# Kernel tuning notes

Hardware: AMD Instinct MI355X
Metric: run time of the kernel (lower is better)

## Reference

```python
import jax, jax.numpy as jnp
import numpy as np

N, C, H, W = 4, 128, 128, 128
G, K, PAD, DIL = 4, 3, 1, 1
P = K * K
HID = 4 * C
EPS = 1e-6


def ln(x, w, b):
    m = jnp.mean(x, -1, keepdims=True)
    v = jnp.mean((x - m) ** 2, -1, keepdims=True)
    return (x - m) * jax.lax.rsqrt(v + EPS) * w + b


def linear(x, w, b):
    return x @ w.T + b


def grid_sample_zeros(img, grid):
    # img: (B,Hi,Wi,Cc); grid: (B,L,P,2) xy in [-1,1]; bilinear, zeros padding, align_corners=False
    B, Hi, Wi, Cc = img.shape
    gx = (grid[..., 0] + 1.0) * (Wi * 0.5) - 0.5
    gy = (grid[..., 1] + 1.0) * (Hi * 0.5) - 0.5
    x0 = jnp.floor(gx)
    y0 = jnp.floor(gy)
    wx1 = gx - x0
    wy1 = gy - y0
    flat = img.reshape(B, Hi * Wi, Cc)
    Bq, L, Pq = gx.shape

    def tap(yy, xx, wgt):
        valid = (xx >= 0) & (xx <= Wi - 1) & (yy >= 0) & (yy <= Hi - 1)
        idx = (jnp.clip(yy, 0, Hi - 1) * Wi + jnp.clip(xx, 0, Wi - 1)).astype(jnp.int32)
        v = jnp.take_along_axis(flat, idx.reshape(B, L * Pq)[..., None], axis=1)
        return v.reshape(B, L, Pq, Cc) * (wgt * valid)[..., None]

    return (tap(y0, x0, (1 - wx1) * (1 - wy1))
            + tap(y0, x0 + 1, wx1 * (1 - wy1))
            + tap(y0 + 1, x0, (1 - wx1) * wy1)
            + tap(y0 + 1, x0 + 1, wx1 * wy1))


def dcn_core(x, offset, mask):
    # faithful port of dcnv3_core_pytorch (stride=1, offset_scale=1.0)
    n, h, w, c = x.shape
    gc = c // G
    xp = jnp.pad(x, ((0, 0), (PAD, PAD), (PAD, PAD), (0, 0)))
    hi, wi = h + 2 * PAD, w + 2 * PAD
    base = (DIL * (K - 1)) // 2 + 0.5
    ref_y = (base + jnp.arange(h, dtype=jnp.float32)) / hi
    ref_x = (base + jnp.arange(w, dtype=jnp.float32)) / wi
    ref = jnp.stack([jnp.broadcast_to(ref_x[None, :], (h, w)),
                     jnp.broadcast_to(ref_y[:, None], (h, w))], -1)  # (h,w,2) xy
    ks = jnp.arange(K, dtype=jnp.float32) * DIL - (DIL * (K - 1)) // 2
    gxk, gyk = jnp.meshgrid(ks, ks, indexing='ij')  # x slow, y fast (torch meshgrid order)
    grid = jnp.tile(jnp.stack([gxk / wi, gyk / hi], -1).reshape(P, 2), (G, 1))  # (G*P,2)
    sn = jnp.array([wi, hi], jnp.float32)
    loc = ref[None, :, :, None, :] + grid[None, None, None] + offset.reshape(n, h, w, G * P, 2) / sn
    sg = (2.0 * loc - 1.0).reshape(n, h * w, G, P, 2).transpose(0, 2, 1, 3, 4).reshape(n * G, h * w, P, 2)
    img = xp.reshape(n, hi, wi, G, gc).transpose(0, 3, 1, 2, 4).reshape(n * G, hi, wi, gc)
    samp = grid_sample_zeros(img, sg)  # (n*G, h*w, P, gc)
    m = mask.reshape(n, h * w, G, P).transpose(0, 2, 1, 3).reshape(n * G, h * w, P)
    out = jnp.einsum('blpc,blp->blc', samp, m)
    return out.reshape(n, G, h * w, gc).transpose(0, 2, 1, 3).reshape(n, h, w, c)


def dcn_forward(xcl, dw_w, dw_b, dwln_w, dwln_b, off_w, off_b, mask_w, mask_b, outproj_w, outproj_b):
    n, h, w, c = xcl.shape
    y = jax.lax.conv_general_dilated(xcl.transpose(0, 3, 1, 2), dw_w, (1, 1),
                                     ((PAD, PAD), (PAD, PAD)),
                                     dimension_numbers=('NCHW', 'OIHW', 'NCHW'),
                                     feature_group_count=C)
    y = y + dw_b[None, :, None, None]
    x1 = jax.nn.gelu(ln(y.transpose(0, 2, 3, 1), dwln_w, dwln_b), approximate=False)
    offset = linear(x1, off_w, off_b)
    m = jax.nn.softmax(linear(x1, mask_w, mask_b).reshape(n, h, w, G, P), -1).reshape(n, h, w, G * P)
    out = dcn_core(x1, offset, m)
    return linear(out, outproj_w, outproj_b)


def setup_inputs():
    key = jax.random.key(0)
    ks = jax.random.split(key, 8)
    s = 0.02
    return {
        "x": jax.random.normal(ks[0], (N, C, H, W), jnp.float32),
        "norm1_w": jnp.ones((C,), jnp.float32), "norm1_b": jnp.zeros((C,), jnp.float32),
        "dw_w": jax.random.normal(ks[1], (C, 1, K, K), jnp.float32) * 0.1,
        "dw_b": jnp.zeros((C,), jnp.float32),
        "dwln_w": jnp.ones((C,), jnp.float32), "dwln_b": jnp.zeros((C,), jnp.float32),
        "off_w": jax.random.normal(ks[2], (G * P * 2, C), jnp.float32) * 0.05,
        "off_b": jax.random.normal(ks[3], (G * P * 2,), jnp.float32) * 0.5,
        "mask_w": jax.random.normal(ks[4], (G * P, C), jnp.float32) * 0.05,
        "mask_b": jnp.zeros((G * P,), jnp.float32),
        "outproj_w": jax.random.normal(ks[5], (C, C), jnp.float32) * s,
        "outproj_b": jnp.zeros((C,), jnp.float32),
        "norm2_w": jnp.ones((C,), jnp.float32), "norm2_b": jnp.zeros((C,), jnp.float32),
        "fc1_w": jax.random.normal(ks[6], (HID, C), jnp.float32) * s,
        "fc1_b": jnp.zeros((HID,), jnp.float32),
        "fc2_w": jax.random.normal(ks[7], (C, HID), jnp.float32) * s,
        "fc2_b": jnp.zeros((C,), jnp.float32),
    }


def reference(x, norm1_w, norm1_b, dw_w, dw_b, dwln_w, dwln_b, off_w, off_b,
              mask_w, mask_b, outproj_w, outproj_b, norm2_w, norm2_b,
              fc1_w, fc1_b, fc2_w, fc2_b):
    # pre-norm branch (layer_scale=None, post_norm=False, res_post_norm=False, drop_path=Identity)
    xcl = ln(x.transpose(0, 2, 3, 1), norm1_w, norm1_b)  # channels_first -> channels_last LN
    d = dcn_forward(xcl, dw_w, dw_b, dwln_w, dwln_b, off_w, off_b, mask_w, mask_b, outproj_w, outproj_b)
    x = x + d.transpose(0, 3, 1, 2)
    y = ln(x.transpose(0, 2, 3, 1), norm2_w, norm2_b)
    y = linear(jax.nn.gelu(linear(y, fc1_w, fc1_b), approximate=False), fc2_w, fc2_b)
    return x + y.transpose(0, 3, 1, 2)
```

## Files before the change

### kernel.cpp

```cpp
#include <hip/hip_runtime.h>

typedef unsigned short ushort_t;
typedef short short8 __attribute__((ext_vector_type(8)));
typedef float f32x4 __attribute__((ext_vector_type(4)));
typedef ushort_t ushort8v __attribute__((ext_vector_type(8)));
typedef ushort_t ushort4v __attribute__((ext_vector_type(4)));

#define HWsz 16384
#define NHWsz 65536
#define YS 136

__device__ __forceinline__ float b2f(ushort_t u){ return __uint_as_float(((unsigned)u)<<16); }
__device__ __forceinline__ ushort_t f2b(float f){
  unsigned x = __float_as_uint(f);
  x += 0x7fffu + ((x>>16)&1u);
  return (ushort_t)(x>>16);
}
__device__ __forceinline__ float gelu_fast(float x){
  float t = x*x;
  float e = __expf(x*(1.5957691216f + 0.0713548163f*t));
  return x - x*__builtin_amdgcn_rcpf(1.0f + e);
}

#define HSW(p, b) ((p)*1024 + ((b) ^ (((p)&7)<<4)))
#define XSW(p, b) ((p)*256  + ((b) ^ (((p)&7)<<4)))

__global__ __launch_bounds__(256) void kW_cvt(const float* __restrict__ w1, const float* __restrict__ w2,
    const float* __restrict__ offw, const float* __restrict__ maskw, const float* __restrict__ dww,
    const float* __restrict__ pw, const float* __restrict__ offb, const float* __restrict__ mb,
    ushort_t* __restrict__ w1b, ushort_t* __restrict__ w2b, ushort_t* __restrict__ owmb,
    float* __restrict__ dwwT, ushort_t* __restrict__ pwh, ushort_t* __restrict__ pwl,
    float* __restrict__ obm){
  int i = blockIdx.x*256 + threadIdx.x;
  w1b[i] = f2b(w1[i]);
  w2b[i] = f2b(w2[i]);
  if (i < 16384){
    int row = i >> 7, k = i & 127;
    float v = 0.f;
    if (row < 72) v = offw[row*128 + k];
    else if (row < 108) v = maskw[(row-72)*128 + k];
    owmb[i] = f2b(v);
    float pv = pw[i];
    ushort_t hi = f2b(pv);
    pwh[i] = hi;
    pwl[i] = f2b(pv - b2f(hi));
  }
  if (i < 1152){
    int k = i >> 7, c = i & 127;
    dwwT[i] = dww[c*9 + k];
  }
  if (i < 128){
    obm[i] = (i < 72) ? offb[i] : ((i < 108) ? mb[i-72] : 0.f);
  }
}

__global__ __launch_bounds__(256) void kA_ln1(const float* __restrict__ x,
    const float* __restrict__ w, const float* __restrict__ b,
    ushort_t* __restrict__ xcl){
  __shared__ float tile[128*66];
  __shared__ float psum[256], psq[256];
  __shared__ float ms[64], rs[64];
  int t = threadIdx.x;
  int pos0 = blockIdx.x * 64;
  int n = pos0 >> 14, hw0 = pos0 & 16383;
  const float* xb = x + (size_t)n*128*HWsz + hw0;
  for (int i=0;i<32;i++){
    int e = i*256+t;
    int c = e>>6, p = e&63;
    tile[c*66+p] = xb[(size_t)c*HWsz + p];
  }
  __syncthreads();
  {
    int part = t>>6, p = t&63;
    float s=0.f, q=0.f;
    for (int c=part*32; c<part*32+32; c++){ float v = tile[c*66+p]; s+=v; q+=v*v; }
    psum[part*64+p]=s; psq[part*64+p]=q;
  }
  __syncthreads();
  if (t<64){
    float s=psum[t]+psum[64+t]+psum[128+t]+psum[192+t];
    float q=psq[t]+psq[64+t]+psq[128+t]+psq[192+t];
    float m = s*(1.0f/128.0f);
    float v = q*(1.0f/128.0f)-m*m;
    ms[t]=m; rs[t]=rsqrtf(v+1e-6f);
  }
  __syncthreads();
  for (int i=0;i<32;i++){
    int e = i*256+t;
    int p = e>>7, c = e&127;
    float v = (tile[c*66+p]-ms[p])*rs[p]*w[c]+b[c];
    xcl[(size_t)(pos0+p)*128 + c] = f2b(v);
  }
}

__global__ __launch_bounds__(256) void kB_dw(const ushort_t* __restrict__ xcl,
    const float* __restrict__ dwwT, const float* __restrict__ dwb,
    const float* __restrict__ lnw, const float* __restrict__ lnb,
    ushort_t* __restrict__ x1){
  __shared__ float partS[16*17], partQ[16*17];
  __shared__ float ms[16], rs[16];
  int t = threadIdx.x;
  int pos0 = blockIdx.x*16;
  int n = pos0>>14, hw0 = pos0&16383, h = hw0>>7, w0 = hw0&127;
  int pp = t>>4, l = t&15, ch0 = l*8;
  int w = w0 + pp;
  float acc[8];
  {
    float4 b0 = *(const float4*)(dwb + ch0);
    float4 b1 = *(const float4*)(dwb + ch0 + 4);
    acc[0]=b0.x; acc[1]=b0.y; acc[2]=b0.z; acc[3]=b0.w;
    acc[4]=b1.x; acc[5]=b1.y; acc[6]=b1.z; acc[7]=b1.w;
  }
  #pragma unroll
  for (int kh=0; kh<3; kh++){
    int hy = h + kh - 1;
    if ((unsigned)hy < 128u){
      #pragma unroll
      for (int kw=0; kw<3; kw++){
        int wx = w + kw - 1;
        if ((unsigned)wx < 128u){
          ushort8v xv = *(const ushort8v*)(xcl + ((size_t)(n*16384 + hy*128 + wx))*128 + ch0);
          const float* wr = dwwT + (kh*3+kw)*128 + ch0;
          float4 w0v = *(const float4*)(wr);
          float4 w1v = *(const float4*)(wr+4);
          acc[0] += b2f(xv[0])*w0v.x; acc[1] += b2f(xv[1])*w0v.y;
          acc[2] += b2f(xv[2])*w0v.z; acc[3] += b2f(xv[3])*w0v.w;
          acc[4] += b2f(xv[4])*w1v.x; acc[5] += b2f(xv[5])*w1v.y;
          acc[6] += b2f(xv[6])*w1v.z; acc[7] += b2f(xv[7])*w1v.w;
        }
      }
    }
  }
  {
    float s=0.f, q=0.f;
    #pragma unroll
    for (int j=0;j<8;j++){ s+=acc[j]; q+=acc[j]*acc[j]; }
    partS[pp*17+l]=s; partQ[pp*17+l]=q;
  }
  __syncthreads();
  {
    int p = t>>4, j = t&15;
    float s = partS[p*17+j];
    float q = partQ[p*17+j];
    s += __shfl_xor(s, 1);  q += __shfl_xor(q, 1);
    s += __shfl_xor(s, 2);  q += __shfl_xor(q, 2);
    s += __shfl_xor(s, 4);  q += __shfl_xor(q, 4);
    s += __shfl_xor(s, 8);  q += __shfl_xor(q, 8);
    if (j == 0){
      float m = s*(1.0f/128.0f);
      float var = q*(1.0f/128.0f) - m*m;
      ms[p]=m; rs[p]=rsqrtf(var+1e-6f);
    }
  }
  __syncthreads();
  {
    float m = ms[pp], r = rs[pp];
    float4 lw0 = *(const float4*)(lnw + ch0);
    float4 lw1 = *(const float4*)(lnw + ch0 + 4);
    float4 lb0 = *(const float4*)(lnb + ch0);
    float4 lb1 = *(const float4*)(lnb + ch0 + 4);
    float lw[8] = {lw0.x,lw0.y,lw0.z,lw0.w,lw1.x,lw1.y,lw1.z,lw1.w};
    float lb[8] = {lb0.x,lb0.y,lb0.z,lb0.w,lb1.x,lb1.y,lb1.z,lb1.w};
    ushort8v o;
    #pragma unroll
    for (int j=0;j<8;j++){
      float v = (acc[j]-m)*r*lw[j]+lb[j];
      o[j] = f2b(gelu_fast(v));
    }
    *(ushort8v*)(x1 + (size_t)(pos0+pp)*128 + ch0) = o;
  }
}

#define RS 120
__global__ __launch_bounds__(256) void kCD_dcn(const ushort_t* __restrict__ x1,
    const ushort_t* __restrict__ owmb, const float* __restrict__ obm,
    ushort_t* __restrict__ dcnout){
  __shared__ __align__(16) ushort_t xLb[16*YS];
  __shared__ float raw[16*RS];
  __shared__ __align__(16) float descW[576*4];
  __shared__ __align__(16) int   descO[576*4];
  int t = threadIdx.x;
  int pos0 = blockIdx.x*16;
  int n = pos0>>14, hw0 = pos0&16383, h = hw0>>7, w0 = hw0&127;
  const size_t imgbase = (size_t)n*16384*128;

  *(ushort8v*)(xLb + (t>>4)*YS + (t&15)*8) = *(const ushort8v*)(x1 + (size_t)pos0*128 + t*8);
  __syncthreads();

  {
    int wave = t>>6, lane = t&63;
    int ma = lane&15, quad = lane>>4;
    short8 afrag[4];
    #pragma unroll
    for (int ks=0; ks<4; ks++)
      afrag[ks] = *(const short8*)(xLb + ma*YS + ks*32 + quad*8);
    f32x4 acc[2];
    acc[0] = (f32x4){0.f,0.f,0.f,0.f};
    acc[1] = (f32x4){0.f,0.f,0.f,0.f};
    #pragma unroll
    for (int tile=0; tile<2; tile++){
      const ushort_t* brow = owmb + (size_t)(wave*32 + tile*16 + ma)*128 + quad*8;
      #pragma unroll
      for (int ks=0; ks<4; ks++){
        short8 bfrag = *(const short8*)(brow + ks*32);
        acc[tile] = __builtin_amdgcn_mfma_f32_16x16x32_bf16(bfrag, afrag[ks], acc[tile], 0,0,0);
      }
    }
    #pragma unroll
    for (int tile=0; tile<2; tile++){
      int row0 = wave*32 + tile*16 + quad*4;
      if (row0 < 112){
        f32x4 bias4 = *(const f32x4*)(obm + row0);
        f32x4 o;
        #pragma unroll
        for (int r=0;r<4;r++) o[r] = acc[tile][r] + bias4[r];
        *(f32x4*)(raw + ma*RS + row0) = o;
      }
    }
  }
  __syncthreads();

  if (t < 64){
    int p = t>>2, g = t&3;
    float* mr = raw + p*RS + 72 + g*9;
    float mx = -1e30f;
    for (int q=0;q<9;q++) mx = fmaxf(mx, mr[q]);
    float e[9]; float ssum=0.f;
    for (int q=0;q<9;q++){ e[q]=expf(mr[q]-mx); ssum+=e[q]; }
    float inv = 1.0f/ssum;
    for (int q=0;q<9;q++) mr[q] = e[q]*inv;
  }
  __syncthreads();

  for (int it=0; it<3; it++){
    int tid = t + 256*it;
    if (tid < 576){
      int pp = tid/36, rem = tid - pp*36;
      int g = rem/9, p = rem - g*9;
      int i = p/3, j = p - i*3;
      float ox = raw[pp*RS + 2*(g*9+p)];
      float oy = raw[pp*RS + 2*(g*9+p)+1];
      float mval = raw[pp*RS + 72 + g*9 + p];
      float px = (float)(w0 + pp + i - 1) + ox;
      float py = (float)(h + j - 1) + oy;
      float fx0 = floorf(px), fy0 = floorf(py);
      int ix0 = (int)fx0, iy0 = (int)fy0;
      float fx = px - fx0, fy = py - fy0;
      float vx0 = ((unsigned)ix0     < 128u) ? 1.f : 0.f;
      float vx1 = ((unsigned)(ix0+1) < 128u) ? 1.f : 0.f;
      float vy0 = ((unsigned)iy0     < 128u) ? 1.f : 0.f;
      float vy1 = ((unsigned)(iy0+1) < 128u) ? 1.f : 0.f;
      int cx0 = min(max(ix0,0),127), cx1 = min(max(ix0+1,0),127);
      int cy0 = min(max(iy0,0),127), cy1 = min(max(iy0+1,0),127);
      float4 wv;
      wv.x = (1.f-fx)*(1.f-fy)*mval*vx0*vy0;
      wv.y = fx*(1.f-fy)*mval*vx1*vy0;
      wv.z = (1.f-fx)*fy*mval*vx0*vy1;
      wv.w = fx*fy*mval*vx1*vy1;
      int4 ov;
      ov.x = (cy0*128+cx0)*128;
      ov.y = (cy0*128+cx1)*128;
      ov.z = (cy1*128+cx0)*128;
      ov.w = (cy1*128+cx1)*128;
      *(float4*)(descW + tid*4) = wv;
      *(int4*)(descO + tid*4) = ov;
    }
  }
  __syncthreads();

  {
    int pp = t>>4, l = t&15;
    int ch0 = l*8, g = l>>2;
    const ushort_t* ib = x1 + imgbase + ch0;
    float acc[8];
    #pragma unroll
    for (int j=0;j<8;j++) acc[j]=0.f;
    int dbase = pp*36 + g*9;
    #pragma unroll
    for (int p=0;p<9;p++){
      float4 wv = *(const float4*)(descW + (dbase+p)*4);
      int4  ov = *(const int4*)(descO + (dbase+p)*4);
      ushort8v v00 = *(const ushort8v*)(ib + ov.x);
      ushort8v v10 = *(const ushort8v*)(ib + ov.y);
      ushort8v v01 = *(const ushort8v*)(ib + ov.z);
      ushort8v v11 = *(const ushort8v*)(ib + ov.w);
      #pragma unroll
      for (int j=0;j<8;j++){
        float s = wv.x*b2f(v00[j]) + wv.y*b2f(v10[j]) + wv.z*b2f(v01[j]) + wv.w*b2f(v11[j]);
        acc[j] += s;
      }
    }
    ushort8v outv;
    #pragma unroll
    for (int j=0;j<8;j++) outv[j] = f2b(acc[j]);
    *(ushort8v*)(dcnout + (size_t)(pos0+pp)*128 + ch0) = outv;
  }
}

__global__ __launch_bounds__(256, 4) void kEFG(const ushort_t* __restrict__ dcnout,
    const ushort_t* __restrict__ pwh, const ushort_t* __restrict__ pwl,
    const float* __restrict__ pb, const float* __restrict__ x,
    const float* __restrict__ n2w, const float* __restrict__ n2b,
    const ushort_t* __restrict__ w1b, const float* __restrict__ b1,
    const ushort_t* __restrict__ w2b, const float* __restrict__ b2,
    float* __restrict__ out){
  __shared__ __align__(16) char hidb[32*1024];
  __shared__ __align__(16) char xnb[32*256];
  float* partS = (float*)hidb;
  float* partQ = partS + 32*17;
  float* msh   = partQ + 32*17;
  float* rsh   = msh + 32;

  int t = threadIdx.x;
  int pos0 = blockIdx.x*32;
  int n = pos0>>14, hw0 = pos0&16383;
  int wave = t>>6, lane = t&63;
  int ma = lane&15, quad = lane>>4;

  short8 af[2][4];
  #pragma unroll
  for (int mt=0; mt<2; mt++)
    #pragma unroll
    for (int ks=0; ks<4; ks++)
      af[mt][ks] = *(const short8*)(dcnout + (size_t)(pos0+mt*16+ma)*128 + ks*32 + quad*8);

  float res[2][2][4];
  #pragma unroll
  for (int tile=0; tile<2; tile++){
    int c0 = wave*32 + tile*16 + quad*4;
    #pragma unroll
    for (int mt=0; mt<2; mt++){
      int p = mt*16 + ma;
      #pragma unroll
      for (int r=0;r<4;r++)
        res[tile][mt][r] = x[((size_t)(n*128) + c0 + r)*HWsz + hw0 + p];
    }
  }

  f32x4 acc[2][2];
  #pragma unroll
  for (int i=0;i<2;i++){ acc[i][0]=(f32x4){0.f,0.f,0.f,0.f}; acc[i][1]=(f32x4){0.f,0.f,0.f,0.f}; }
  #pragma unroll
  for (int tile=0; tile<2; tile++){
    int c0 = wave*32 + tile*16;
    const ushort_t* bh = pwh + (size_t)(c0 + ma)*128 + quad*8;
    const ushort_t* bl = pwl + (size_t)(c0 + ma)*128 + quad*8;
    #pragma unroll
    for (int ks=0; ks<4; ks++){
      short8 bfh = *(const short8*)(bh + ks*32);
      short8 bfl = *(const short8*)(bl + ks*32);
      #pragma unroll
      for (int mt=0; mt<2; mt++){
        acc[tile][mt] = __builtin_amdgcn_mfma_f32_16x16x32_bf16(bfh, af[mt][ks], acc[tile][mt], 0,0,0);
        acc[tile][mt] = __builtin_amdgcn_mfma_f32_16x16x32_bf16(bfl, af[mt][ks], acc[tile][mt], 0,0,0);
      }
    }
  }

  float vb[2][2][4];
  float sAcc[2], qAcc[2];
  sAcc[0]=0.f; sAcc[1]=0.f; qAcc[0]=0.f; qAcc[1]=0.f;
  #pragma unroll
  for (int tile=0; tile<2; tile++){
    int c0 = wave*32 + tile*16 + quad*4;
    f32x4 bias4 = *(const f32x4*)(pb + c0);
    #pragma unroll
    for (int mt=0; mt<2; mt++){
      #pragma unroll
      for (int r=0;r<4;r++){
        float v = acc[tile][mt][r] + bias4[r] + res[tile][mt][r];
        float vv = b2f(f2b(v));
        vb[tile][mt][r] = vv;
        sAcc[mt] += vv; qAcc[mt] += vv*vv;
      }
    }
  }
  #pragma unroll
  for (int mt=0; mt<2; mt++){
    int p = mt*16 + ma;
    partS[p*17 + wave*4 + quad] = sAcc[mt];
    partQ[p*17 + wave*4 + quad] = qAcc[mt];
  }
  __syncthreads();
  {
    int p = t>>3, j = t&7;
    float s = partS[p*17 + 2*j] + partS[p*17 + 2*j + 1];
    float q = partQ[p*17 + 2*j] + partQ[p*17 + 2*j + 1];
    s += __shfl_xor(s, 1);  q += __shfl_xor(q, 1);
    s += __shfl_xor(s, 2);  q += __shfl_xor(q, 2);
    s += __shfl_xor(s, 4);  q += __shfl_xor(q, 4);
    if (j == 0){
      float m = s*(1.0f/128.0f);
      float var = q*(1.0f/128.0f) - m*m;
      msh[p] = m; rsh[p] = rsqrtf(var+1e-6f);
    }
  }
  __syncthreads();

  #pragma unroll
  for (int tile=0; tile<2; tile++){
    int c0 = wave*32 + tile*16 + quad*4;
    f32x4 w4 = *(const f32x4*)(n2w + c0);
    f32x4 b4 = *(const f32x4*)(n2b + c0);
    #pragma unroll
    for (int mt=0; mt<2; mt++){
      int p = mt*16 + ma;
      float m = msh[p], r = rsh[p];
      ushort4v nv;
      #pragma unroll
      for (int rr=0;rr<4;rr++) nv[rr] = f2b((vb[tile][mt][rr]-m)*r*w4[rr] + b4[rr]);
      *(ushort4v*)(xnb + XSW(p, c0*2)) = nv;
    }
  }
  __syncthreads();

  short8 axf[2][4];
  #pragma unroll
  for (int ks=0; ks<4; ks++)
    #pragma unroll
    for (int mt=0; mt<2; mt++)
      axf[mt][ks] = *(const short8*)(xnb + XSW(mt*16+ma, ks*64 + quad*16));

  int nbase = wave*128;
  const ushort_t* w1base = w1b + (size_t)(nbase + ma)*128 + quad*8;
  short8 wr[3][4];
  #pragma unroll
  for (int tt=0; tt<2; tt++)
    #pragma unroll
    for (int ks=0; ks<4; ks++)
      wr[tt][ks] = *(const short8*)(w1base + tt*2048 + ks*32);
  #pragma unroll
  for (int tile=0; tile<8; tile++){
    if (tile < 6){
      #pragma unroll
      for (int ks=0; ks<4; ks++)
        wr[(tile+2)%3][ks] = *(const short8*)(w1base + (tile+2)*2048 + ks*32);
    }
    f32x4 a0 = (f32x4){0.f,0.f,0.f,0.f};
    f32x4 a1 = (f32x4){0.f,0.f,0.f,0.f};
    #pragma unroll
    for (int ks=0; ks<4; ks++){
      a0 = __builtin_amdgcn_mfma_f32_16x16x32_bf16(wr[tile%3][ks], axf[0][ks], a0, 0,0,0);
      a1 = __builtin_amdgcn_mfma_f32_16x16x32_bf16(wr[tile%3][ks], axf[1][ks], a1, 0,0,0);
    }
    int n0 = nbase + tile*16 + quad*4;
    f32x4 bias4 = *(const f32x4*)(b1 + n0);
    ushort4v hv0, hv1;
    #pragma unroll
    for (int r=0;r<4;r++){
      hv0[r] = f2b(gelu_fast(a0[r] + bias4[r]));
      hv1[r] = f2b(gelu_fast(a1[r] + bias4[r]));
    }
    *(ushort4v*)(hidb + HSW(ma,    n0*2)) = hv0;
    *(ushort4v*)(hidb + HSW(16+ma, n0*2)) = hv1;
  }
  __syncthreads();

  f32x4 acc2[2][2];
  acc2[0][0]=(f32x4){0.f,0.f,0.f,0.f}; acc2[0][1]=(f32x4){0.f,0.f,0.f,0.f};
  acc2[1][0]=(f32x4){0.f,0.f,0.f,0.f}; acc2[1][1]=(f32x4){0.f,0.f,0.f,0.f};
  const ushort_t* wb0 = w2b + (size_t)(wave*32 + ma)*512 + quad*8;
  const ushort_t* wb1 = wb0 + 16*512;
  short8 wq0[4], wq1[4];
  #pragma unroll
  for (int i=0;i<4;i++){
    wq0[i] = *(const short8*)(wb0 + i*32);
    wq1[i] = *(const short8*)(wb1 + i*32);
  }
  short8 hq0[2], hq1[2];
  hq0[0] = *(const short8*)(hidb + HSW(ma,    quad*16));
  hq1[0] = *(const short8*)(hidb + HSW(16+ma, quad*16));
  hq0[1] = *(const short8*)(hidb + HSW(ma,    64 + quad*16));
  hq1[1] = *(const short8*)(hidb + HSW(16+ma, 64 + quad*16));
  #pragma unroll
  for (int ks=0; ks<16; ks++){
    short8 wc0 = wq0[ks&3], wc1 = wq1[ks&3];
    short8 hc0 = hq0[ks&1], hc1 = hq1[ks&1];
    if (ks < 12){
      wq0[ks&3] = *(const short8*)(wb0 + (ks+4)*32);
      wq1[ks&3] = *(const short8*)(wb1 + (ks+4)*32);
    }
    if (ks < 14){
      hq0[ks&1] = *(const short8*)(hidb + HSW(ma,    (ks+2)*64 + quad*16));
      hq1[ks&1] = *(const short8*)(hidb + HSW(16+ma, (ks+2)*64 + quad*16));
    }
    acc2[0][0] = __builtin_amdgcn_mfma_f32_16x16x32_bf16(wc0, hc0, acc2[0][0], 0,0,0);
    acc2[0][1] = __builtin_amdgcn_mfma_f32_16x16x32_bf16(wc0, hc1, acc2[0][1], 0,0,0);
    acc2[1][0] = __builtin_amdgcn_mfma_f32_16x16x32_bf16(wc1, hc0, acc2[1][0], 0,0,0);
    acc2[1][1] = __builtin_amdgcn_mfma_f32_16x16x32_bf16(wc1, hc1, acc2[1][1], 0,0,0);
  }

  #pragma unroll
  for (int tile=0; tile<2; tile++){
    int c0 = wave*32 + tile*16 + quad*4;
    f32x4 bias4 = *(const f32x4*)(b2 + c0);
    #pragma unroll
    for (int mt=0; mt<2; mt++){
      int p = mt*16 + ma;
      #pragma unroll
      for (int r=0;r<4;r++){
        float v = acc2[tile][mt][r] + bias4[r] + vb[tile][mt][r];
        out[((size_t)(n*128) + c0 + r)*HWsz + hw0 + p] = v;
      }
    }
  }
}

extern "C" void kernel_launch(void* const* d_in, const int* in_sizes, int n_in,
                              void* d_out, int out_size, void* d_ws, size_t ws_size,
                              hipStream_t stream){
  const float* x     = (const float*)d_in[0];
  const float* n1w   = (const float*)d_in[1];
  const float* n1b   = (const float*)d_in[2];
  const float* dww   = (const float*)d_in[3];
  const float* dwb   = (const float*)d_in[4];
  const float* dwlnw = (const float*)d_in[5];
  const float* dwlnb = (const float*)d_in[6];
  const float* offw  = (const float*)d_in[7];
  const float* offb  = (const float*)d_in[8];
  const float* maskw = (const float*)d_in[9];
  const float* maskb = (const float*)d_in[10];
  const float* pw    = (const float*)d_in[11];
  const float* pb    = (const float*)d_in[12];
  const float* n2w   = (const float*)d_in[13];
  const float* n2b   = (const float*)d_in[14];
  const float* w1    = (const float*)d_in[15];
  const float* b1    = (const float*)d_in[16];
  const float* w2    = (const float*)d_in[17];
  const float* b2    = (const float*)d_in[18];

  char* wsb = (char*)d_ws;
  ushort_t* R0   = (ushort_t*)(wsb);
  ushort_t* R1   = (ushort_t*)(wsb + (16u<<20));
  ushort_t* w1b  = (ushort_t*)(wsb + (32u<<20));
  ushort_t* w2b  = (ushort_t*)(wsb + (32u<<20) + (128u<<10));
  ushort_t* owmb = (ushort_t*)(wsb + (32u<<20) + (256u<<10));
  ushort_t* pwh  = (ushort_t*)(wsb + (32u<<20) + (288u<<10));
  ushort_t* pwl  = (ushort_t*)(wsb + (32u<<20) + (320u<<10));
  float*    dwwT = (float*)(wsb + (32u<<20) + (352u<<10));
  float*    obm  = (float*)(wsb + (32u<<20) + (358u<<10));
  float* out = (float*)d_out;

  hipLaunchKernelGGL(kW_cvt,  dim3(256),   dim3(256), 0, stream, w1, w2, offw, maskw, dww, pw, offb, maskb, w1b, w2b, owmb, dwwT, pwh, pwl, obm);
  hipLaunchKernelGGL(kA_ln1,  dim3(1024),  dim3(256), 0, stream, x, n1w, n1b, R0);
  hipLaunchKernelGGL(kB_dw,   dim3(4096),  dim3(256), 0, stream, R0, dwwT, dwb, dwlnw, dwlnb, R1);
  hipLaunchKernelGGL(kCD_dcn, dim3(4096),  dim3(256), 0, stream, R1, owmb, obm, R0);
  hipLaunchKernelGGL(kEFG,    dim3(2048),  dim3(256), 0, stream, R0, pwh, pwl, pb, x, n2w, n2b, w1b, b1, w2b, b2, out);
}
```

Measured before the change: 277.9 us.

## Split MLP hidden dimension into halves to halve LDS and raise occupancy

The fused outproj+LN+MLP kernel now computes the 512-wide hidden activation in two 256-wide halves, so the shared hidden buffer shrinks from 32KB to 16KB and fc2 accumulates across halves. The residual is kept packed as bf16 and loaded lazily, and the explicit software prefetch of weights is removed, all to cut registers and LDS so launch bounds can go from 4 to 6 blocks per CU. This adds an extra barrier per half and loses the manual load pipelining, which may expose global load latency.

```diff
diff --git a/kernel.cpp b/kernel.cpp
--- a/kernel.cpp
+++ b/kernel.cpp
@@ -22,8 +22,8 @@
   return x - x*__builtin_amdgcn_rcpf(1.0f + e);
 }
 
-#define HSW(p, b) ((p)*1024 + ((b) ^ (((p)&7)<<4)))
-#define XSW(p, b) ((p)*256  + ((b) ^ (((p)&7)<<4)))
+#define H16(p, b) ((p)*512 + ((b) ^ (((p)&7)<<4)))
+#define XSW(p, b) ((p)*256 + ((b) ^ (((p)&7)<<4)))
 
 __global__ __launch_bounds__(256) void kW_cvt(const float* __restrict__ w1, const float* __restrict__ w2,
     const float* __restrict__ offw, const float* __restrict__ maskw, const float* __restrict__ dww,
@@ -297,14 +297,14 @@
   }
 }
 
-__global__ __launch_bounds__(256, 4) void kEFG(const ushort_t* __restrict__ dcnout,
+__global__ __launch_bounds__(256, 6) void kEFG(const ushort_t* __restrict__ dcnout,
     const ushort_t* __restrict__ pwh, const ushort_t* __restrict__ pwl,
     const float* __restrict__ pb, const float* __restrict__ x,
     const float* __restrict__ n2w, const float* __restrict__ n2b,
     const ushort_t* __restrict__ w1b, const float* __restrict__ b1,
     const ushort_t* __restrict__ w2b, const float* __restrict__ b2,
     float* __restrict__ out){
-  __shared__ __align__(16) char hidb[32*1024];
+  __shared__ __align__(16) char hidb[16*1024];
   __shared__ __align__(16) char xnb[32*256];
   float* partS = (float*)hidb;
   float* partQ = partS + 32*17;
@@ -324,19 +324,6 @@
     for (int ks=0; ks<4; ks++)
       af[mt][ks] = *(const short8*)(dcnout + (size_t)(pos0+mt*16+ma)*128 + ks*32 + quad*8);
 
-  float res[2][2][4];
-  #pragma unroll
-  for (int tile=0; tile<2; tile++){
-    int c0 = wave*32 + tile*16 + quad*4;
-    #pragma unroll
-    for (int mt=0; mt<2; mt++){
-      int p = mt*16 + ma;
-      #pragma unroll
-      for (int r=0;r<4;r++)
-        res[tile][mt][r] = x[((size_t)(n*128) + c0 + r)*HWsz + hw0 + p];
-    }
-  }
-
   f32x4 acc[2][2];
   #pragma unroll
   for (int i=0;i<2;i++){ acc[i][0]=(f32x4){0.f,0.f,0.f,0.f}; acc[i][1]=(f32x4){0.f,0.f,0.f,0.f}; }
@@ -357,7 +344,7 @@
     }
   }
 
-  float vb[2][2][4];
+  ushort4v vbp[2][2];
   float sAcc[2], qAcc[2];
   sAcc[0]=0.f; sAcc[1]=0.f; qAcc[0]=0.f; qAcc[1]=0.f;
   #pragma unroll
@@ -366,13 +353,18 @@
     f32x4 bias4 = *(const f32x4*)(pb + c0);
     #pragma unroll
     for (int mt=0; mt<2; mt++){
+      int p = mt*16 + ma;
+      ushort4v ov;
       #pragma unroll
       for (int r=0;r<4;r++){
-        float v = acc[tile][mt][r] + bias4[r] + res[tile][mt][r];
-        float vv = b2f(f2b(v));
-        vb[tile][mt][r] = vv;
+        float res = x[((size_t)(n*128) + c0 + r)*HWsz + hw0 + p];
+        float v = acc[tile][mt][r] + bias4[r] + res;
+        ushort_t ub = f2b(v);
+        ov[r] = ub;
+        float vv = b2f(ub);
         sAcc[mt] += vv; qAcc[mt] += vv*vv;
       }
+      vbp[tile][mt] = ov;
     }
   }
   #pragma unroll
@@ -408,7 +400,7 @@
       float m = msh[p], r = rsh[p];
       ushort4v nv;
       #pragma unroll
-      for (int rr=0;rr<4;rr++) nv[rr] = f2b((vb[tile][mt][rr]-m)*r*w4[rr] + b4[rr]);
+      for (int rr=0;rr<4;rr++) nv[rr] = f2b((b2f(vbp[tile][mt][rr])-m)*r*w4[rr] + b4[rr]);
       *(ushort4v*)(xnb + XSW(p, c0*2)) = nv;
     }
   }
@@ -420,74 +412,54 @@
     #pragma unroll
     for (int mt=0; mt<2; mt++)
       axf[mt][ks] = *(const short8*)(xnb + XSW(mt*16+ma, ks*64 + quad*16));
-
-  int nbase = wave*128;
-  const ushort_t* w1base = w1b + (size_t)(nbase + ma)*128 + quad*8;
-  short8 wr[3][4];
-  #pragma unroll
-  for (int tt=0; tt<2; tt++)
-    #pragma unroll
-    for (int ks=0; ks<4; ks++)
-      wr[tt][ks] = *(const short8*)(w1base + tt*2048 + ks*32);
-  #pragma unroll
-  for (int tile=0; tile<8; tile++){
-    if (tile < 6){
-      #pragma unroll
-      for (int ks=0; ks<4; ks++)
-        wr[(tile+2)%3][ks] = *(const short8*)(w1base + (tile+2)*2048 + ks*32);
-    }
-    f32x4 a0 = (f32x4){0.f,0.f,0.f,0.f};
-    f32x4 a1 = (f32x4){0.f,0.f,0.f,0.f};
-    #pragma unroll
-    for (int ks=0; ks<4; ks++){
-      a0 = __builtin_amdgcn_mfma_f32_16x16x32_bf16(wr[tile%3][ks], axf[0][ks], a0, 0,0,0);
-      a1 = __builtin_amdgcn_mfma_f32_16x16x32_bf16(wr[tile%3][ks], axf[1][ks], a1, 0,0,0);
-    }
-    int n0 = nbase + tile*16 + quad*4;
-    f32x4 bias4 = *(const f32x4*)(b1 + n0);
-    ushort4v hv0, hv1;
-    #pragma unroll
-    for (int r=0;r<4;r++){
-      hv0[r] = f2b(gelu_fast(a0[r] + bias4[r]));
-      hv1[r] = f2b(gelu_fast(a1[r] + bias4[r]));
-    }
-    *(ushort4v*)(hidb + HSW(ma,    n0*2)) = hv0;
-    *(ushort4v*)(hidb + HSW(16+ma, n0*2)) = hv1;
-  }
-  __syncthreads();
 
   f32x4 acc2[2][2];
   acc2[0][0]=(f32x4){0.f,0.f,0.f,0.f}; acc2[0][1]=(f32x4){0.f,0.f,0.f,0.f};
   acc2[1][0]=(f32x4){0.f,0.f,0.f,0.f}; acc2[1][1]=(f32x4){0.f,0.f,0.f,0.f};
-  const ushort_t* wb0 = w2b + (size_t)(wave*32 + ma)*512 + quad*8;
-  const ushort_t* wb1 = wb0 + 16*512;
-  short8 wq0[4], wq1[4];
-  #pragma unroll
-  for (int i=0;i<4;i++){
-    wq0[i] = *(const short8*)(wb0 + i*32);
-    wq1[i] = *(const short8*)(wb1 + i*32);
-  }
-  short8 hq0[2], hq1[2];
-  hq0[0] = *(const short8*)(hidb + HSW(ma,    quad*16));
-  hq1[0] = *(const short8*)(hidb + HSW(16+ma, quad*16));
-  hq0[1] = *(const short8*)(hidb + HSW(ma,    64 + quad*16));
-  hq1[1] = *(const short8*)(hidb + HSW(16+ma, 64 + quad*16));
-  #pragma unroll
-  for (int ks=0; ks<16; ks++){
-    short8 wc0 = wq0[ks&3], wc1 = wq1[ks&3];
-    short8 hc0 = hq0[ks&1], hc1 = hq1[ks&1];
-    if (ks < 12){
-      wq0[ks&3] = *(const short8*)(wb0 + (ks+4)*32);
-      wq1[ks&3] = *(const short8*)(wb1 + (ks+4)*32);
-    }
-    if (ks < 14){
-      hq0[ks&1] = *(const short8*)(hidb + HSW(ma,    (ks+2)*64 + quad*16));
-      hq1[ks&1] = *(const short8*)(hidb + HSW(16+ma, (ks+2)*64 + quad*16));
-    }
-    acc2[0][0] = __builtin_amdgcn_mfma_f32_16x16x32_bf16(wc0, hc0, acc2[0][0], 0,0,0);
-    acc2[0][1] = __builtin_amdgcn_mfma_f32_16x16x32_bf16(wc0, hc1, acc2[0][1], 0,0,0);
-    acc2[1][0] = __builtin_amdgcn_mfma_f32_16x16x32_bf16(wc1, hc0, acc2[1][0], 0,0,0);
-    acc2[1][1] = __builtin_amdgcn_mfma_f32_16x16x32_bf16(wc1, hc1, acc2[1][1], 0,0,0);
+
+  #pragma unroll
+  for (int half=0; half<2; half++){
+    #pragma unroll
+    for (int tt=0; tt<4; tt++){
+      int n0g = half*256 + wave*64 + tt*16;
+      const ushort_t* brow = w1b + (size_t)(n0g + ma)*128 + quad*8;
+      short8 bf[4];
+      #pragma unroll
+      for (int ks=0; ks<4; ks++) bf[ks] = *(const short8*)(brow + ks*32);
+      f32x4 a0 = (f32x4){0.f,0.f,0.f,0.f};
+      f32x4 a1 = (f32x4){0.f,0.f,0.f,0.f};
+      #pragma unroll
+      for (int ks=0; ks<4; ks++){
+        a0 = __builtin_amdgcn_mfma_f32_16x16x32_bf16(bf[ks], axf[0][ks], a0, 0,0,0);
+        a1 = __builtin_amdgcn_mfma_f32_16x16x32_bf16(bf[ks], axf[1][ks], a1, 0,0,0);
+      }
+      f32x4 bias4 = *(const f32x4*)(b1 + n0g + quad*4);
+      ushort4v hv0, hv1;
+      #pragma unroll
+      for (int r=0;r<4;r++){
+        hv0[r] = f2b(gelu_fast(a0[r] + bias4[r]));
+        hv1[r] = f2b(gelu_fast(a1[r] + bias4[r]));
+      }
+      int nloc = wave*64 + tt*16 + quad*4;
+      *(ushort4v*)(hidb + H16(ma,    nloc*2)) = hv0;
+      *(ushort4v*)(hidb + H16(16+ma, nloc*2)) = hv1;
+    }
+    __syncthreads();
+
+    const ushort_t* wb0 = w2b + (size_t)(wave*32 + ma)*512 + half*256 + quad*8;
+    const ushort_t* wb1 = wb0 + 16*512;
+    #pragma unroll
+    for (int ksl=0; ksl<8; ksl++){
+      short8 wc0 = *(const short8*)(wb0 + ksl*32);
+      short8 wc1 = *(const short8*)(wb1 + ksl*32);
+      short8 hc0 = *(const short8*)(hidb + H16(ma,    ksl*64 + quad*16));
+      short8 hc1 = *(const short8*)(hidb + H16(16+ma, ksl*64 + quad*16));
+      acc2[0][0] = __builtin_amdgcn_mfma_f32_16x16x32_bf16(wc0, hc0, acc2[0][0], 0,0,0);
+      acc2[0][1] = __builtin_amdgcn_mfma_f32_16x16x32_bf16(wc0, hc1, acc2[0][1], 0,0,0);
+      acc2[1][0] = __builtin_amdgcn_mfma_f32_16x16x32_bf16(wc1, hc0, acc2[1][0], 0,0,0);
+      acc2[1][1] = __builtin_amdgcn_mfma_f32_16x16x32_bf16(wc1, hc1, acc2[1][1], 0,0,0);
+    }
+    if (half == 0) __syncthreads();
   }
 
   #pragma unroll
@@ -499,7 +471,7 @@
       int p = mt*16 + ma;
       #pragma unroll
       for (int r=0;r<4;r++){
-        float v = acc2[tile][mt][r] + bias4[r] + vb[tile][mt][r];
+        float v = acc2[tile][mt][r] + bias4[r] + b2f(vbp[tile][mt][r]);
         out[((size_t)(n*128) + c0 + r)*HWsz + hw0 + p] = v;
       }
     }
```

Result: slower. 299.1 us (+7.6%).
